# Optimization experiments

Measured on AMD Instinct MI355X. Metric: run time of the kernel, lower is better.

## Reference

```python
import jax, jax.numpy as jnp
import numpy as np

N_IN, N_OUT = 8192, 4096
INIT_TAU = 2.0
V_TH = 1.0
SLOPE = 10.0  # fast-sigmoid surrogate slope


def setup_inputs() -> dict:
    key = jax.random.key(0)
    k1, k2, k3, k4, k5 = jax.random.split(key, 5)
    x = jax.random.normal(k1, (N_IN,), jnp.float32)
    W = jax.random.normal(k2, (N_IN, N_OUT), jnp.float32) / np.sqrt(N_IN).astype(np.float32)
    u = jax.random.normal(k3, (N_OUT,), jnp.float32)
    E = jax.random.normal(k4, (N_IN, N_OUT), jnp.float32) * 0.1
    R_hat = jax.random.normal(k5, (N_IN, N_OUT), jnp.float32) * 0.1
    g_bar = jnp.zeros((N_OUT,), jnp.float32)
    ratio = jnp.zeros((1,), jnp.float32)
    return {"x": x, "W": W, "u": u, "E": E, "R_hat": R_hat, "g_bar": g_bar, "ratio": ratio}


def _step(x, W, u, E, R_hat, g_bar, ratio):
    # One OTPE timestep. SNN: Dense connection + LIF with soft (detached) reset.
    sig_tau = jax.nn.sigmoid(jnp.float32(INIT_TAU))
    u_pre = sig_tau * u + x @ W                       # [n_out]
    s = (u_pre >= V_TH).astype(jnp.float32)           # spike (heaviside fwd)
    sg = 1.0 / (1.0 + SLOPE * jnp.abs(u_pre - V_TH)) ** 2  # surrogate d s/d u_pre
    u_new = u_pre - s * V_TH                          # soft reset (s detached)
    # analytic per-step VJPs of sum(s) and sum(u) wrt (u_prev, theta):
    ds_du_prev = sg * sig_tau                         # [n_out]
    ds_dtheta_cur = x[:, None] * sg[None, :]          # [n_in, n_out]
    # du_cur_du_prev = sig_tau ; du_cur_dtheta_cur = outer(x, ones)
    ds_dtheta = ds_du_prev[None, :] * E + ds_dtheta_cur   # map_s over pytree
    E_new = sig_tau * E + x[:, None]                      # map_u over pytree
    R_new = sig_tau * R_hat + ds_dtheta                   # map_r
    r0 = sig_tau * ratio                               # [1]
    ratio_new = r0 + 1.0
    r = r0 / ratio_new
    g_bar_new = r * g_bar + (1.0 - r) * (ds_du_prev / sig_tau)
    return s, u_new, E_new, R_new, g_bar_new, ratio_new


def reference(x, W, u, E, R_hat, g_bar, ratio):
    # returns (s, carry_u, carry_E, carry_R_hat, carry_g_bar, carry_ratio)
    return _step(x, W, u, E, R_hat, g_bar, ratio)
```

## Files before the change

kernel.cpp:

```cpp
#include <hip/hip_runtime.h>


#define SIG_TAU 0.8807970779778823f

constexpr int N_IN  = 8192;
constexpr int N_OUT = 4096;
constexpr int NCG   = N_OUT / 4;
constexpr int ROWS_PER_CHUNK = 64;

constexpr size_t OFF_S     = 0;
constexpr size_t OFF_U     = (size_t)N_OUT;
constexpr size_t OFF_E     = (size_t)2 * N_OUT;
constexpr size_t OFF_R     = OFF_E + (size_t)N_IN * N_OUT;
constexpr size_t OFF_G     = OFF_R + (size_t)N_IN * N_OUT;
constexpr size_t OFF_RATIO = OFF_G + (size_t)N_OUT;

__global__ __launch_bounds__(256) void matvec_partial(
    const float* __restrict__ x, const float4* __restrict__ W4,
    float* __restrict__ acc) {
    const int cg   = blockIdx.x * 256 + threadIdx.x;
    const int row0 = blockIdx.y * ROWS_PER_CHUNK;
    float4 a = make_float4(0.f, 0.f, 0.f, 0.f);
#pragma unroll 8
    for (int r = 0; r < ROWS_PER_CHUNK; ++r) {
        const float  xv = x[row0 + r];
        const float4 w  = W4[(size_t)(row0 + r) * NCG + cg];
        a.x = fmaf(xv, w.x, a.x);
        a.y = fmaf(xv, w.y, a.y);
        a.z = fmaf(xv, w.z, a.z);
        a.w = fmaf(xv, w.w, a.w);
    }
    float* dst = acc + (size_t)cg * 4;
    atomicAdd(dst + 0, a.x);
    atomicAdd(dst + 1, a.y);
    atomicAdd(dst + 2, a.z);
    atomicAdd(dst + 3, a.w);
}

__global__ __launch_bounds__(256) void finalize(
    const float* __restrict__ acc, const float* __restrict__ u,
    const float* __restrict__ g_bar, const float* __restrict__ ratio,
    float* __restrict__ out, float* __restrict__ sg_ws) {
    const int j = blockIdx.x * 256 + threadIdx.x;
    if (j >= N_OUT) return;
    const float u_pre = fmaf(SIG_TAU, u[j], acc[j]);
    const float s     = (u_pre >= 1.0f) ? 1.0f : 0.0f;
    const float t     = 1.0f / fmaf(10.0f, fabsf(u_pre - 1.0f), 1.0f);
    const float sg    = t * t;
    const float u_new = u_pre - s;

    const float r0        = SIG_TAU * ratio[0];
    const float ratio_new = r0 + 1.0f;
    const float r         = r0 / ratio_new;
    const float g_new = fmaf(r, g_bar[j], (1.0f - r) * sg);

    out[OFF_S + j] = s;
    out[OFF_U + j] = u_new;
    out[OFF_G + j] = g_new;
    sg_ws[j] = sg;
    if (j == 0) out[OFF_RATIO] = ratio_new;
}

__global__ __launch_bounds__(256) void elemwise(
    const float* __restrict__ x, const float4* __restrict__ E4,
    const float4* __restrict__ R4, const float4* __restrict__ sg4,
    float4* __restrict__ Enew4, float4* __restrict__ Rnew4) {
    const size_t total  = (size_t)N_IN * NCG;
    const size_t stride = (size_t)gridDim.x * blockDim.x;
    for (size_t idx = (size_t)blockIdx.x * blockDim.x + threadIdx.x;
         idx < total; idx += stride) {
        const int i  = (int)(idx >> 10);
        const int cg = (int)(idx & (NCG - 1));
        const float  xv = x[i];
        const float4 s4 = sg4[cg];
        const float4 e  = E4[idx];
        const float4 rr = R4[idx];
        float4 en, rn;
        en.x = fmaf(SIG_TAU, e.x, xv);
        en.y = fmaf(SIG_TAU, e.y, xv);
        en.z = fmaf(SIG_TAU, e.z, xv);
        en.w = fmaf(SIG_TAU, e.w, xv);
        rn.x = fmaf(s4.x, en.x, SIG_TAU * rr.x);
        rn.y = fmaf(s4.y, en.y, SIG_TAU * rr.y);
        rn.z = fmaf(s4.z, en.z, SIG_TAU * rr.z);
        rn.w = fmaf(s4.w, en.w, SIG_TAU * rr.w);
        Enew4[idx] = en;
        Rnew4[idx] = rn;
    }
}

extern "C" void kernel_launch(void* const* d_in, const int* in_sizes, int n_in,
                              void* d_out, int out_size, void* d_ws, size_t ws_size,
                              hipStream_t stream) {
    const float* x     = (const float*)d_in[0];
    const float* W     = (const float*)d_in[1];
    const float* u     = (const float*)d_in[2];
    const float* E     = (const float*)d_in[3];
    const float* R_hat = (const float*)d_in[4];
    const float* g_bar = (const float*)d_in[5];
    const float* ratio = (const float*)d_in[6];
    float* out = (float*)d_out;

    float* acc = (float*)d_ws;
    float* sg  = acc + N_OUT;

    hipMemsetAsync(acc, 0, N_OUT * sizeof(float), stream);

    dim3 g1(NCG / 256, N_IN / ROWS_PER_CHUNK);
    matvec_partial<<<g1, 256, 0, stream>>>(x, (const float4*)W, acc);

    finalize<<<N_OUT / 256, 256, 0, stream>>>(acc, u, g_bar, ratio, out, sg);

    elemwise<<<4096, 256, 0, stream>>>(
        x, (const float4*)E, (const float4*)R_hat, (const float4*)sg,
        (float4*)(out + OFF_E), (float4*)(out + OFF_R));
}
```

Baseline: 529.1 us.

## Replace atomic matvec reduction with partial buffers and use nontemporal elementwise streaming

The matvec kernel now writes per-chunk partial sums to a workspace buffer instead of issuing float atomics, and finalize reduces the 128 partials per column. This also removes the memset launch. The elementwise kernel uses a fixed 8-iteration unrolled loop with nontemporal loads and stores for E and R, to cut cache pollution on the large streaming traffic. The trade-off is an extra 2MB partial buffer that is written and then read back, and finalize becomes a serial 128-step reduction per thread.

```diff
diff --git a/kernel.cpp b/kernel.cpp
--- a/kernel.cpp
+++ b/kernel.cpp
@@ -1,12 +1,15 @@
 #include <hip/hip_runtime.h>
 
+
+typedef float f4 __attribute__((ext_vector_type(4)));
 
 #define SIG_TAU 0.8807970779778823f
 
 constexpr int N_IN  = 8192;
 constexpr int N_OUT = 4096;
 constexpr int NCG   = N_OUT / 4;
-constexpr int ROWS_PER_CHUNK = 64;
+constexpr int RPC   = 64;
+constexpr int NCHUNK = N_IN / RPC;
 
 constexpr size_t OFF_S     = 0;
 constexpr size_t OFF_U     = (size_t)N_OUT;
@@ -16,34 +19,31 @@
 constexpr size_t OFF_RATIO = OFF_G + (size_t)N_OUT;
 
 __global__ __launch_bounds__(256) void matvec_partial(
-    const float* __restrict__ x, const float4* __restrict__ W4,
-    float* __restrict__ acc) {
+    const float* __restrict__ x, const f4* __restrict__ W4,
+    f4* __restrict__ part) {
     const int cg   = blockIdx.x * 256 + threadIdx.x;
-    const int row0 = blockIdx.y * ROWS_PER_CHUNK;
-    float4 a = make_float4(0.f, 0.f, 0.f, 0.f);
+    const int row0 = blockIdx.y * RPC;
+    f4 a = {0.f, 0.f, 0.f, 0.f};
 #pragma unroll 8
-    for (int r = 0; r < ROWS_PER_CHUNK; ++r) {
-        const float  xv = x[row0 + r];
-        const float4 w  = W4[(size_t)(row0 + r) * NCG + cg];
-        a.x = fmaf(xv, w.x, a.x);
-        a.y = fmaf(xv, w.y, a.y);
-        a.z = fmaf(xv, w.z, a.z);
-        a.w = fmaf(xv, w.w, a.w);
+    for (int r = 0; r < RPC; ++r) {
+        const float xv = x[row0 + r];
+        const f4    w  = W4[(size_t)(row0 + r) * NCG + cg];
+        a += w * xv;
     }
-    float* dst = acc + (size_t)cg * 4;
-    atomicAdd(dst + 0, a.x);
-    atomicAdd(dst + 1, a.y);
-    atomicAdd(dst + 2, a.z);
-    atomicAdd(dst + 3, a.w);
+    part[(size_t)blockIdx.y * NCG + cg] = a;
 }
 
 __global__ __launch_bounds__(256) void finalize(
-    const float* __restrict__ acc, const float* __restrict__ u,
+    const float* __restrict__ part, const float* __restrict__ u,
     const float* __restrict__ g_bar, const float* __restrict__ ratio,
     float* __restrict__ out, float* __restrict__ sg_ws) {
     const int j = blockIdx.x * 256 + threadIdx.x;
-    if (j >= N_OUT) return;
-    const float u_pre = fmaf(SIG_TAU, u[j], acc[j]);
+    float acc = 0.f;
+#pragma unroll 8
+    for (int c = 0; c < NCHUNK; ++c)
+        acc += part[(size_t)c * N_OUT + j];
+
+    const float u_pre = fmaf(SIG_TAU, u[j], acc);
     const float s     = (u_pre >= 1.0f) ? 1.0f : 0.0f;
     const float t     = 1.0f / fmaf(10.0f, fabsf(u_pre - 1.0f), 1.0f);
     const float sg    = t * t;
@@ -62,30 +62,24 @@
 }
 
 __global__ __launch_bounds__(256) void elemwise(
-    const float* __restrict__ x, const float4* __restrict__ E4,
-    const float4* __restrict__ R4, const float4* __restrict__ sg4,
-    float4* __restrict__ Enew4, float4* __restrict__ Rnew4) {
-    const size_t total  = (size_t)N_IN * NCG;
-    const size_t stride = (size_t)gridDim.x * blockDim.x;
-    for (size_t idx = (size_t)blockIdx.x * blockDim.x + threadIdx.x;
-         idx < total; idx += stride) {
+    const float* __restrict__ x, const f4* __restrict__ E4,
+    const f4* __restrict__ R4, const f4* __restrict__ sg4,
+    f4* __restrict__ Enew4, f4* __restrict__ Rnew4) {
+    const size_t base    = (size_t)blockIdx.x * 256 + threadIdx.x;
+    constexpr size_t STR = (size_t)4096 * 256;
+#pragma unroll
+    for (int k = 0; k < 8; ++k) {
+        const size_t idx = base + (size_t)k * STR;
         const int i  = (int)(idx >> 10);
         const int cg = (int)(idx & (NCG - 1));
-        const float  xv = x[i];
-        const float4 s4 = sg4[cg];
-        const float4 e  = E4[idx];
-        const float4 rr = R4[idx];
-        float4 en, rn;
-        en.x = fmaf(SIG_TAU, e.x, xv);
-        en.y = fmaf(SIG_TAU, e.y, xv);
-        en.z = fmaf(SIG_TAU, e.z, xv);
-        en.w = fmaf(SIG_TAU, e.w, xv);
-        rn.x = fmaf(s4.x, en.x, SIG_TAU * rr.x);
-        rn.y = fmaf(s4.y, en.y, SIG_TAU * rr.y);
-        rn.z = fmaf(s4.z, en.z, SIG_TAU * rr.z);
-        rn.w = fmaf(s4.w, en.w, SIG_TAU * rr.w);
-        Enew4[idx] = en;
-        Rnew4[idx] = rn;
+        const float xv  = x[i];
+        const f4    sgv = sg4[cg];
+        const f4 e  = __builtin_nontemporal_load(&E4[idx]);
+        const f4 rr = __builtin_nontemporal_load(&R4[idx]);
+        const f4 en = e * SIG_TAU + xv;
+        const f4 rn = rr * SIG_TAU + sgv * en;
+        __builtin_nontemporal_store(en, &Enew4[idx]);
+        __builtin_nontemporal_store(rn, &Rnew4[idx]);
     }
 }
 
@@ -101,17 +95,15 @@
     const float* ratio = (const float*)d_in[6];
     float* out = (float*)d_out;
 
-    float* acc = (float*)d_ws;
-    float* sg  = acc + N_OUT;
+    float* part = (float*)d_ws;
+    float* sg   = part + (size_t)NCHUNK * N_OUT;
 
-    hipMemsetAsync(acc, 0, N_OUT * sizeof(float), stream);
+    dim3 g1(NCG / 256, NCHUNK);
+    matvec_partial<<<g1, 256, 0, stream>>>(x, (const f4*)W, (f4*)part);
 
-    dim3 g1(NCG / 256, N_IN / ROWS_PER_CHUNK);
-    matvec_partial<<<g1, 256, 0, stream>>>(x, (const float4*)W, acc);
-
-    finalize<<<N_OUT / 256, 256, 0, stream>>>(acc, u, g_bar, ratio, out, sg);
+    finalize<<<N_OUT / 256, 256, 0, stream>>>(part, u, g_bar, ratio, out, sg);
 
     elemwise<<<4096, 256, 0, stream>>>(
-        x, (const float4*)E, (const float4*)R_hat, (const float4*)sg,
-        (float4*)(out + OFF_E), (float4*)(out + OFF_R));
+        x, (const f4*)E, (const f4*)R_hat, (const f4*)sg,
+        (f4*)(out + OFF_E), (f4*)(out + OFF_R));
 }
```

Measured after the change: 536.3 us. About the same (+1.4%).
